# Kernel tuning notes

Measured on AMD Instinct MI355X. Metric: run time of the kernel, lower is better.

Reference implementation:

```python
import jax, jax.numpy as jnp
import numpy as np

DIM = 64
CTX = 64
HID = 512
K = 16          # n_bins
TB = 5.0        # tail_bound
N_T = DIM // 2  # n_transform_dims (mask_even=True -> odd indices transformed)
N_P = 3 * K - 1 # params per transformed dim
BATCH = 65536


def setup_inputs() -> dict:
    key = jax.random.key(0)
    ks = jax.random.split(key, 9)
    s = 0.05
    return {
        "x": jax.random.normal(ks[0], (BATCH, DIM), jnp.float32),
        "context": jax.random.normal(ks[1], (BATCH, CTX), jnp.float32),
        "W1": jax.random.normal(ks[2], (DIM + CTX, HID), jnp.float32) * s,
        "b1": jnp.zeros((HID,), jnp.float32),
        "W2": jax.random.normal(ks[3], (HID, HID), jnp.float32) * s,
        "b2": jnp.zeros((HID,), jnp.float32),
        "W3": jax.random.normal(ks[4], (HID, N_T * N_P), jnp.float32) * s,
        "b3": jnp.zeros((N_T * N_P,), jnp.float32),
    }


def _spline_forward(x, raw_params):
    # x: (batch, d); raw_params: (batch, d, 3K-1)
    B = TB
    Wb = jax.nn.softmax(raw_params[..., :K], axis=-1) * (2 * B)       # bin widths
    Hb = jax.nn.softmax(raw_params[..., K:2 * K], axis=-1) * (2 * B)  # bin heights
    D = jax.nn.softplus(raw_params[..., 2 * K:])                      # (batch,d,K-1)
    ones = jnp.ones(D.shape[:-1] + (1,), D.dtype)
    D = jnp.concatenate([ones, D, ones], axis=-1)                     # (batch,d,K+1)

    cumw = jnp.cumsum(Wb, axis=-1) - B
    cumh = jnp.cumsum(Hb, axis=-1) - B
    negB = jnp.full(cumw.shape[:-1] + (1,), -B, cumw.dtype)
    cumw = jnp.concatenate([negB, cumw], axis=-1)                     # (batch,d,K+1)
    cumh = jnp.concatenate([negB, cumh], axis=-1)

    x_c = jnp.clip(x, -B + 1e-06, B - 1e-06)
    # torch.searchsorted left on cumw[...,1:]: count of knots strictly < x
    bin_idx = jnp.sum(cumw[..., 1:] < x_c[..., None], axis=-1)
    bin_idx = jnp.clip(bin_idx, 0, K - 1)[..., None]                  # (batch,d,1)

    take = lambda a: jnp.take_along_axis(a, bin_idx, axis=-1)[..., 0]
    w_k = take(Wb)
    h_k = take(Hb)
    d_k = take(D[..., :-1])
    d_kp1 = take(D[..., 1:])
    cw_k = take(cumw)
    ch_k = take(cumh)

    xi = jnp.clip((x_c - cw_k) / w_k, 0.0, 1.0)
    om = 1.0 - xi
    numerator = h_k * (d_k * xi * xi + 2 * xi * om)
    denominator = d_k + (d_kp1 + d_k - 2) * xi * om
    y = ch_k + numerator / (denominator + 1e-08)
    log_deriv = jnp.log(
        h_k * h_k * (d_kp1 * xi * xi + 2 * xi * om + d_k * om * om)
        / (denominator * denominator * w_k + 1e-08) + 1e-08
    )
    return y, log_deriv


def reference(x, context, W1, b1, W2, b2, W3, b3):
    mask = jnp.zeros((DIM,), x.dtype).at[::2].set(1.0)
    x_masked = x * mask
    inp = jnp.concatenate([x_masked, context], axis=-1)
    h = jax.nn.silu(inp @ W1 + b1)
    h = jax.nn.silu(h @ W2 + b2)
    raw = (h @ W3 + b3).reshape(-1, N_T, N_P)
    x_t = x[:, 1::2]  # mask==0 columns (odd indices)
    y_t, log_det = _spline_forward(x_t, raw)
    y = x.at[:, 1::2].set(y_t)
    return y, jnp.sum(log_det, axis=-1)
```

## Files before the change

kernel.cpp:

```cpp
#include <hip/hip_runtime.h>


typedef _Float16 v8h __attribute__((ext_vector_type(8)));
typedef float v4f __attribute__((ext_vector_type(4)));

#define ROWS_PER_BLOCK 32
#define NBLOCKS (65536 / ROWS_PER_BLOCK)
#define NWAVES 16

#define SMEM_BYTES 147456
#define S_INPLO 8192
#define S_H1HI  16384
#define S_H1LO  49152
#define S_H2HI  81920
#define S_H2LO  114688
#define RAW_STRIDE 388

#define LO_SCALE 2048.f
#define LO_INV   (1.f / 2048.f)

__device__ __forceinline__ void split2(float x, _Float16& hi, _Float16& lo) {
    _Float16 h = (_Float16)x;
    hi = h;
    lo = (_Float16)((x - (float)h) * LO_SCALE);
}
__device__ __forceinline__ float silu_f(float v) {
    return v / (1.f + __expf(-v));
}
__device__ __forceinline__ float softplus_f(float v) {
    return v > 15.f ? v : __logf(1.f + __expf(v));
}

__global__ void nscl_prep_frag(const float* __restrict__ src,
                               _Float16* __restrict__ hi, _Float16* __restrict__ lo,
                               int K, int N) {
    int idx = blockIdx.x * blockDim.x + threadIdx.x;
    if (idx >= N * K) return;
    const int e    = idx & 7;
    const int lane = (idx >> 3) & 63;
    const int rem  = idx >> 9;
    const int KS   = K >> 5;
    const int ks   = rem % KS;
    const int j    = rem / KS;
    const int n = j * 16 + (lane & 15);
    const int k = ks * 32 + ((lane >> 4) << 3) + e;
    split2(src[k * N + n], hi[idx], lo[idx]);
}

template<int KS, int NPAIRS, bool DOSILU>
__device__ __forceinline__ void gemm_phase(const _Float16* __restrict__ sAhi,
                                           const _Float16* __restrict__ sAlo,
                                           const _Float16* __restrict__ Bhi,
                                           const _Float16* __restrict__ Blo,
                                           const float* __restrict__ bias,
                                           _Float16* __restrict__ sOutHi,
                                           _Float16* __restrict__ sOutLo,
                                           int wave, int lane) {
    const int lr = lane & 15;
    const int rb = (lane >> 4) << 2;

    for (int p = wave; p < NPAIRS; p += NWAVES) {
        const int j0 = p * 2;
        v4f m00 = {0,0,0,0}, m10 = {0,0,0,0}, m01 = {0,0,0,0}, m11 = {0,0,0,0};
        v4f c00 = {0,0,0,0}, c10 = {0,0,0,0}, c01 = {0,0,0,0}, c11 = {0,0,0,0};
        #pragma unroll
        for (int ks = 0; ks < KS; ++ks) {
            const int ab = (ks * 64 + lane) * 8;
            v8h a0h = *(const v8h*)(sAhi + ab);
            v8h a0l = *(const v8h*)(sAlo + ab);
            v8h a1h = *(const v8h*)(sAhi + KS * 512 + ab);
            v8h a1l = *(const v8h*)(sAlo + KS * 512 + ab);
            const int bo0 = ((j0 * KS + ks) * 64 + lane) * 8;
            const int bo1 = (((j0 + 1) * KS + ks) * 64 + lane) * 8;
            v8h b0h = *(const v8h*)(Bhi + bo0);
            v8h b0l = *(const v8h*)(Blo + bo0);
            v8h b1h = *(const v8h*)(Bhi + bo1);
            v8h b1l = *(const v8h*)(Blo + bo1);
            m00 = __builtin_amdgcn_mfma_f32_16x16x32_f16(a0h, b0h, m00, 0, 0, 0);
            m10 = __builtin_amdgcn_mfma_f32_16x16x32_f16(a1h, b0h, m10, 0, 0, 0);
            m01 = __builtin_amdgcn_mfma_f32_16x16x32_f16(a0h, b1h, m01, 0, 0, 0);
            m11 = __builtin_amdgcn_mfma_f32_16x16x32_f16(a1h, b1h, m11, 0, 0, 0);
            c00 = __builtin_amdgcn_mfma_f32_16x16x32_f16(a0h, b0l, c00, 0, 0, 0);
            c00 = __builtin_amdgcn_mfma_f32_16x16x32_f16(a0l, b0h, c00, 0, 0, 0);
            c10 = __builtin_amdgcn_mfma_f32_16x16x32_f16(a1h, b0l, c10, 0, 0, 0);
            c10 = __builtin_amdgcn_mfma_f32_16x16x32_f16(a1l, b0h, c10, 0, 0, 0);
            c01 = __builtin_amdgcn_mfma_f32_16x16x32_f16(a0h, b1l, c01, 0, 0, 0);
            c01 = __builtin_amdgcn_mfma_f32_16x16x32_f16(a0l, b1h, c01, 0, 0, 0);
            c11 = __builtin_amdgcn_mfma_f32_16x16x32_f16(a1h, b1l, c11, 0, 0, 0);
            c11 = __builtin_amdgcn_mfma_f32_16x16x32_f16(a1l, b1h, c11, 0, 0, 0);
        }
        #pragma unroll
        for (int jj = 0; jj < 2; ++jj) {
            const int C   = (j0 + jj) * 16 + lr;
            const int ks2 = C >> 5, g2 = (C >> 3) & 3, e2 = C & 7;
            const float bv = bias[C];
            const v4f mm0 = jj ? m01 : m00;
            const v4f mm1 = jj ? m11 : m10;
            const v4f cc0 = jj ? c01 : c00;
            const v4f cc1 = jj ? c11 : c10;
            #pragma unroll
            for (int r = 0; r < 4; ++r) {
                float v0 = mm0[r] + cc0[r] * LO_INV + bv;
                float v1 = mm1[r] + cc1[r] * LO_INV + bv;
                if (DOSILU) { v0 = silu_f(v0); v1 = silu_f(v1); }
                const int off0 = (ks2 * 64 + g2 * 16 + rb + r) * 8 + e2;
                const int off1 = ((16 + ks2) * 64 + g2 * 16 + rb + r) * 8 + e2;
                split2(v0, sOutHi[off0], sOutLo[off0]);
                split2(v1, sOutHi[off1], sOutLo[off1]);
            }
        }
    }
}

__device__ __forceinline__ void gemm3_chunk(const _Float16* __restrict__ sH2Hi,
                                            const _Float16* __restrict__ sH2Lo,
                                            const _Float16* __restrict__ W3hi,
                                            const _Float16* __restrict__ W3lo,
                                            const float* __restrict__ b3,
                                            float* __restrict__ sRaw,
                                            int t0, int wave, int lane) {
    const int lr = lane & 15;
    const int rb = (lane >> 4) << 2;

    for (int tt = wave; tt < 24; tt += NWAVES) {
        const int jt = t0 + tt;
        v4f m0 = {0,0,0,0}, m1 = {0,0,0,0};
        v4f cc0 = {0,0,0,0}, cc1 = {0,0,0,0};
        #pragma unroll
        for (int ks = 0; ks < 16; ++ks) {
            const int ab = (ks * 64 + lane) * 8;
            v8h a0h = *(const v8h*)(sH2Hi + ab);
            v8h a0l = *(const v8h*)(sH2Lo + ab);
            v8h a1h = *(const v8h*)(sH2Hi + 8192 + ab);
            v8h a1l = *(const v8h*)(sH2Lo + 8192 + ab);
            const int bo = ((jt * 16 + ks) * 64 + lane) * 8;
            v8h bh = *(const v8h*)(W3hi + bo);
            v8h bl = *(const v8h*)(W3lo + bo);
            m0  = __builtin_amdgcn_mfma_f32_16x16x32_f16(a0h, bh, m0, 0, 0, 0);
            m1  = __builtin_amdgcn_mfma_f32_16x16x32_f16(a1h, bh, m1, 0, 0, 0);
            cc0 = __builtin_amdgcn_mfma_f32_16x16x32_f16(a0h, bl, cc0, 0, 0, 0);
            cc0 = __builtin_amdgcn_mfma_f32_16x16x32_f16(a0l, bh, cc0, 0, 0, 0);
            cc1 = __builtin_amdgcn_mfma_f32_16x16x32_f16(a1h, bl, cc1, 0, 0, 0);
            cc1 = __builtin_amdgcn_mfma_f32_16x16x32_f16(a1l, bh, cc1, 0, 0, 0);
        }
        const int col  = jt * 16 + lr;
        const int lcol = tt * 16 + lr;
        const float bv = b3[col];
        #pragma unroll
        for (int r = 0; r < 4; ++r) {
            sRaw[(rb + r) * RAW_STRIDE + lcol]      = m0[r] + cc0[r] * LO_INV + bv;
            sRaw[(16 + rb + r) * RAW_STRIDE + lcol] = m1[r] + cc1[r] * LO_INV + bv;
        }
    }
}

__global__ __launch_bounds__(1024, 4)
void nscl_fused(const float* __restrict__ xp, const float* __restrict__ ctxp,
                const float* __restrict__ b1, const float* __restrict__ b2,
                const float* __restrict__ b3,
                const _Float16* __restrict__ W1Thi, const _Float16* __restrict__ W1Tlo,
                const _Float16* __restrict__ W2Thi, const _Float16* __restrict__ W2Tlo,
                const _Float16* __restrict__ W3Thi, const _Float16* __restrict__ W3Tlo,
                float* __restrict__ outY, float* __restrict__ outLD) {
    __shared__ __align__(16) char smem[SMEM_BYTES];
    _Float16* sInpHi = (_Float16*)smem;
    _Float16* sInpLo = (_Float16*)(smem + S_INPLO);
    _Float16* sH1Hi  = (_Float16*)(smem + S_H1HI);
    _Float16* sH1Lo  = (_Float16*)(smem + S_H1LO);
    _Float16* sH2Hi  = (_Float16*)(smem + S_H2HI);
    _Float16* sH2Lo  = (_Float16*)(smem + S_H2LO);
    float*    sRaw   = (float*)smem;

    const int tid  = threadIdx.x;
    const int lane = tid & 63;
    const int wave = tid >> 6;
    const int row0 = blockIdx.x * ROWS_PER_BLOCK;

    for (int idx = tid; idx < ROWS_PER_BLOCK * 128; idx += 1024) {
        const int e  = idx & 7;
        const int l  = (idx >> 3) & 63;
        const int ks = (idx >> 9) & 3;
        const int mt = idx >> 11;
        const int row = mt * 16 + (l & 15);
        const int c   = ks * 32 + ((l >> 4) << 3) + e;
        float v;
        if (c < 64) v = (c & 1) ? 0.f : xp[(row0 + row) * 64 + c];
        else        v = ctxp[(row0 + row) * 64 + (c - 64)];
        split2(v, sInpHi[idx], sInpLo[idx]);
    }
    __syncthreads();

    gemm_phase<4, 16, true>(sInpHi, sInpLo, W1Thi, W1Tlo, b1,
                            sH1Hi, sH1Lo, wave, lane);
    __syncthreads();
    gemm_phase<16, 16, true>(sH1Hi, sH1Lo, W2Thi, W2Tlo, b2,
                             sH2Hi, sH2Lo, wave, lane);
    __syncthreads();

    const float TB = 5.0f;
    float ldacc = 0.f;
    const int r  = (tid < 256) ? (tid >> 3) : 0;
    const int tl = tid & 7;
    const int t0s[4] = {0, 23, 47, 70};

    #pragma unroll 1
    for (int ch = 0; ch < 4; ++ch) {
        gemm3_chunk(sH2Hi, sH2Lo, W3Thi, W3Tlo, b3, sRaw, t0s[ch], wave, lane);
        __syncthreads();

        if (tid < 256) {
            const int t = ch * 8 + tl;
            const int g = row0 + r;
            const float* pr = sRaw + r * RAW_STRIDE + ((ch & 1) ? 8 : 0) + tl * 47;

            float mw = -1e30f, mh = -1e30f;
            #pragma unroll
            for (int i = 0; i < 16; ++i) {
                mw = fmaxf(mw, pr[i]);
                mh = fmaxf(mh, pr[16 + i]);
            }
            float wv[16], hv[16];
            float sw = 0.f, sh = 0.f;
            #pragma unroll
            for (int i = 0; i < 16; ++i) {
                wv[i] = __expf(pr[i] - mw);       sw += wv[i];
                hv[i] = __expf(pr[16 + i] - mh);  sh += hv[i];
            }
            const float scw = 10.f / sw;
            const float sch = 10.f / sh;

            const float xt = xp[g * 64 + 2 * t + 1];
            const float xc = fminf(fmaxf(xt, -TB + 1e-6f), TB - 1e-6f);

            float cum = -TB; int cnt = 0;
            #pragma unroll
            for (int i = 0; i < 16; ++i) {
                cum += wv[i] * scw;
                cnt += (cum < xc) ? 1 : 0;
            }
            const int bin = cnt > 15 ? 15 : cnt;

            float w_k = 0.f, cw_k = 0.f, h_k = 0.f, ch_k = 0.f;
            float cw = -TB, chh = -TB;
            #pragma unroll
            for (int i = 0; i < 16; ++i) {
                const float wi = wv[i] * scw;
                const float hi = hv[i] * sch;
                if (i == bin) { w_k = wi; cw_k = cw; h_k = hi; ch_k = chh; }
                cw += wi; chh += hi;
            }

            const float d_k  = (bin == 0)  ? 1.f : softplus_f(pr[31 + bin]);
            const float d_k1 = (bin == 15) ? 1.f : softplus_f(pr[32 + bin]);

            float xi = (xc - cw_k) / w_k;
            xi = fminf(fmaxf(xi, 0.f), 1.f);
            const float om = 1.f - xi;
            const float num = h_k * (d_k * xi * xi + 2.f * xi * om);
            const float den = d_k + (d_k1 + d_k - 2.f) * xi * om;
            const float yv  = ch_k + num / (den + 1e-8f);
            const float dv  = h_k * h_k * (d_k1 * xi * xi + 2.f * xi * om + d_k * om * om)
                              / (den * den * w_k + 1e-8f) + 1e-8f;

            float v = __logf(dv);
            v += __shfl_xor(v, 1);
            v += __shfl_xor(v, 2);
            v += __shfl_xor(v, 4);
            ldacc += v;

            outY[g * 64 + 2 * t]     = xp[g * 64 + 2 * t];
            outY[g * 64 + 2 * t + 1] = yv;
        }
        __syncthreads();
    }

    if (tid < 256 && tl == 0) outLD[row0 + r] = ldacc;
}

extern "C" void kernel_launch(void* const* d_in, const int* in_sizes, int n_in,
                              void* d_out, int out_size, void* d_ws, size_t ws_size,
                              hipStream_t stream) {
    (void)in_sizes; (void)n_in; (void)out_size; (void)ws_size;
    const float* x   = (const float*)d_in[0];
    const float* ctx = (const float*)d_in[1];
    const float* W1  = (const float*)d_in[2];
    const float* b1  = (const float*)d_in[3];
    const float* W2  = (const float*)d_in[4];
    const float* b2  = (const float*)d_in[5];
    const float* W3  = (const float*)d_in[6];
    const float* b3  = (const float*)d_in[7];

    _Float16* base = (_Float16*)d_ws;
    _Float16* W1Thi = base;
    _Float16* W1Tlo = base + 65536;
    _Float16* W2Thi = base + 131072;
    _Float16* W2Tlo = base + 393216;
    _Float16* W3Thi = base + 655360;
    _Float16* W3Tlo = base + 1425408;

    nscl_prep_frag<<<(512 * 128 + 255) / 256, 256, 0, stream>>>(W1, W1Thi, W1Tlo, 128, 512);
    nscl_prep_frag<<<(512 * 512 + 255) / 256, 256, 0, stream>>>(W2, W2Thi, W2Tlo, 512, 512);
    nscl_prep_frag<<<(512 * 1504 + 255) / 256, 256, 0, stream>>>(W3, W3Thi, W3Tlo, 512, 1504);

    float* outY  = (float*)d_out;
    float* outLD = outY + 65536 * 64;

    nscl_fused<<<NBLOCKS, 1024, 0, stream>>>(x, ctx, b1, b2, b3,
                                             W1Thi, W1Tlo, W2Thi, W2Tlo, W3Thi, W3Tlo,
                                             outY, outLD);
}
```

Baseline: 640.1 us.

## Use single-tile GEMM waves and recompute spline exps to cut register pressure

GEMM1/GEMM2 now give each wave one 16-column tile instead of a pair, halving accumulators and B-fragment registers per wave. Each B load is now reused across only two row tiles instead of four MFMA products, and all 32 tiles map onto 16 waves in two loop iterations. The spline stage no longer keeps 32-element exp arrays in registers and instead recomputes the exps in each pass, trading extra transcendental work for fewer live registers. The chunk offset table is replaced by an arithmetic expression that yields the same values.

```diff
diff --git a/kernel.cpp b/kernel.cpp
--- a/kernel.cpp
+++ b/kernel.cpp
@@ -3,6 +3,8 @@
 
 typedef _Float16 v8h __attribute__((ext_vector_type(8)));
 typedef float v4f __attribute__((ext_vector_type(4)));
+
+#define MFMA16(a, b, c) __builtin_amdgcn_mfma_f32_16x16x32_f16((a), (b), (c), 0, 0, 0)
 
 #define ROWS_PER_BLOCK 32
 #define NBLOCKS (65536 / ROWS_PER_BLOCK)
@@ -47,7 +49,7 @@
     split2(src[k * N + n], hi[idx], lo[idx]);
 }
 
-template<int KS, int NPAIRS, bool DOSILU>
+template<int KS, int NTILES, bool DOSILU>
 __device__ __forceinline__ void gemm_phase(const _Float16* __restrict__ sAhi,
                                            const _Float16* __restrict__ sAlo,
                                            const _Float16* __restrict__ Bhi,
@@ -59,10 +61,9 @@
     const int lr = lane & 15;
     const int rb = (lane >> 4) << 2;
 
-    for (int p = wave; p < NPAIRS; p += NWAVES) {
-        const int j0 = p * 2;
-        v4f m00 = {0,0,0,0}, m10 = {0,0,0,0}, m01 = {0,0,0,0}, m11 = {0,0,0,0};
-        v4f c00 = {0,0,0,0}, c10 = {0,0,0,0}, c01 = {0,0,0,0}, c11 = {0,0,0,0};
+    for (int p = wave; p < NTILES; p += NWAVES) {
+        v4f m0 = {0,0,0,0}, m1 = {0,0,0,0};
+        v4f c0 = {0,0,0,0}, c1 = {0,0,0,0};
         #pragma unroll
         for (int ks = 0; ks < KS; ++ks) {
             const int ab = (ks * 64 + lane) * 8;
@@ -70,44 +71,28 @@
             v8h a0l = *(const v8h*)(sAlo + ab);
             v8h a1h = *(const v8h*)(sAhi + KS * 512 + ab);
             v8h a1l = *(const v8h*)(sAlo + KS * 512 + ab);
-            const int bo0 = ((j0 * KS + ks) * 64 + lane) * 8;
-            const int bo1 = (((j0 + 1) * KS + ks) * 64 + lane) * 8;
-            v8h b0h = *(const v8h*)(Bhi + bo0);
-            v8h b0l = *(const v8h*)(Blo + bo0);
-            v8h b1h = *(const v8h*)(Bhi + bo1);
-            v8h b1l = *(const v8h*)(Blo + bo1);
-            m00 = __builtin_amdgcn_mfma_f32_16x16x32_f16(a0h, b0h, m00, 0, 0, 0);
-            m10 = __builtin_amdgcn_mfma_f32_16x16x32_f16(a1h, b0h, m10, 0, 0, 0);
-            m01 = __builtin_amdgcn_mfma_f32_16x16x32_f16(a0h, b1h, m01, 0, 0, 0);
-            m11 = __builtin_amdgcn_mfma_f32_16x16x32_f16(a1h, b1h, m11, 0, 0, 0);
-            c00 = __builtin_amdgcn_mfma_f32_16x16x32_f16(a0h, b0l, c00, 0, 0, 0);
-            c00 = __builtin_amdgcn_mfma_f32_16x16x32_f16(a0l, b0h, c00, 0, 0, 0);
-            c10 = __builtin_amdgcn_mfma_f32_16x16x32_f16(a1h, b0l, c10, 0, 0, 0);
-            c10 = __builtin_amdgcn_mfma_f32_16x16x32_f16(a1l, b0h, c10, 0, 0, 0);
-            c01 = __builtin_amdgcn_mfma_f32_16x16x32_f16(a0h, b1l, c01, 0, 0, 0);
-            c01 = __builtin_amdgcn_mfma_f32_16x16x32_f16(a0l, b1h, c01, 0, 0, 0);
-            c11 = __builtin_amdgcn_mfma_f32_16x16x32_f16(a1h, b1l, c11, 0, 0, 0);
-            c11 = __builtin_amdgcn_mfma_f32_16x16x32_f16(a1l, b1h, c11, 0, 0, 0);
-        }
-        #pragma unroll
-        for (int jj = 0; jj < 2; ++jj) {
-            const int C   = (j0 + jj) * 16 + lr;
-            const int ks2 = C >> 5, g2 = (C >> 3) & 3, e2 = C & 7;
-            const float bv = bias[C];
-            const v4f mm0 = jj ? m01 : m00;
-            const v4f mm1 = jj ? m11 : m10;
-            const v4f cc0 = jj ? c01 : c00;
-            const v4f cc1 = jj ? c11 : c10;
-            #pragma unroll
-            for (int r = 0; r < 4; ++r) {
-                float v0 = mm0[r] + cc0[r] * LO_INV + bv;
-                float v1 = mm1[r] + cc1[r] * LO_INV + bv;
-                if (DOSILU) { v0 = silu_f(v0); v1 = silu_f(v1); }
-                const int off0 = (ks2 * 64 + g2 * 16 + rb + r) * 8 + e2;
-                const int off1 = ((16 + ks2) * 64 + g2 * 16 + rb + r) * 8 + e2;
-                split2(v0, sOutHi[off0], sOutLo[off0]);
-                split2(v1, sOutHi[off1], sOutLo[off1]);
-            }
+            const int bo = ((p * KS + ks) * 64 + lane) * 8;
+            v8h bh = *(const v8h*)(Bhi + bo);
+            v8h bl = *(const v8h*)(Blo + bo);
+            m0 = MFMA16(a0h, bh, m0);
+            m1 = MFMA16(a1h, bh, m1);
+            c0 = MFMA16(a0h, bl, c0);
+            c0 = MFMA16(a0l, bh, c0);
+            c1 = MFMA16(a1h, bl, c1);
+            c1 = MFMA16(a1l, bh, c1);
+        }
+        const int C   = p * 16 + lr;
+        const int ks2 = C >> 5, g2 = (C >> 3) & 3, e2 = C & 7;
+        const float bv = bias[C];
+        #pragma unroll
+        for (int rr = 0; rr < 4; ++rr) {
+            float v0 = m0[rr] + c0[rr] * LO_INV + bv;
+            float v1 = m1[rr] + c1[rr] * LO_INV + bv;
+            if (DOSILU) { v0 = silu_f(v0); v1 = silu_f(v1); }
+            const int off0 = (ks2 * 64 + g2 * 16 + rb + rr) * 8 + e2;
+            const int off1 = ((16 + ks2) * 64 + g2 * 16 + rb + rr) * 8 + e2;
+            split2(v0, sOutHi[off0], sOutLo[off0]);
+            split2(v1, sOutHi[off1], sOutLo[off1]);
         }
     }
 }
@@ -125,7 +110,7 @@
     for (int tt = wave; tt < 24; tt += NWAVES) {
         const int jt = t0 + tt;
         v4f m0 = {0,0,0,0}, m1 = {0,0,0,0};
-        v4f cc0 = {0,0,0,0}, cc1 = {0,0,0,0};
+        v4f c0 = {0,0,0,0}, c1 = {0,0,0,0};
         #pragma unroll
         for (int ks = 0; ks < 16; ++ks) {
             const int ab = (ks * 64 + lane) * 8;
@@ -136,20 +121,20 @@
             const int bo = ((jt * 16 + ks) * 64 + lane) * 8;
             v8h bh = *(const v8h*)(W3hi + bo);
             v8h bl = *(const v8h*)(W3lo + bo);
-            m0  = __builtin_amdgcn_mfma_f32_16x16x32_f16(a0h, bh, m0, 0, 0, 0);
-            m1  = __builtin_amdgcn_mfma_f32_16x16x32_f16(a1h, bh, m1, 0, 0, 0);
-            cc0 = __builtin_amdgcn_mfma_f32_16x16x32_f16(a0h, bl, cc0, 0, 0, 0);
-            cc0 = __builtin_amdgcn_mfma_f32_16x16x32_f16(a0l, bh, cc0, 0, 0, 0);
-            cc1 = __builtin_amdgcn_mfma_f32_16x16x32_f16(a1h, bl, cc1, 0, 0, 0);
-            cc1 = __builtin_amdgcn_mfma_f32_16x16x32_f16(a1l, bh, cc1, 0, 0, 0);
+            m0 = MFMA16(a0h, bh, m0);
+            m1 = MFMA16(a1h, bh, m1);
+            c0 = MFMA16(a0h, bl, c0);
+            c0 = MFMA16(a0l, bh, c0);
+            c1 = MFMA16(a1h, bl, c1);
+            c1 = MFMA16(a1l, bh, c1);
         }
         const int col  = jt * 16 + lr;
         const int lcol = tt * 16 + lr;
         const float bv = b3[col];
         #pragma unroll
-        for (int r = 0; r < 4; ++r) {
-            sRaw[(rb + r) * RAW_STRIDE + lcol]      = m0[r] + cc0[r] * LO_INV + bv;
-            sRaw[(16 + rb + r) * RAW_STRIDE + lcol] = m1[r] + cc1[r] * LO_INV + bv;
+        for (int rr = 0; rr < 4; ++rr) {
+            sRaw[(rb + rr) * RAW_STRIDE + lcol]      = m0[rr] + c0[rr] * LO_INV + bv;
+            sRaw[(16 + rb + rr) * RAW_STRIDE + lcol] = m1[rr] + c1[rr] * LO_INV + bv;
         }
     }
 }
@@ -190,10 +175,10 @@
     }
     __syncthreads();
 
-    gemm_phase<4, 16, true>(sInpHi, sInpLo, W1Thi, W1Tlo, b1,
+    gemm_phase<4, 32, true>(sInpHi, sInpLo, W1Thi, W1Tlo, b1,
                             sH1Hi, sH1Lo, wave, lane);
     __syncthreads();
-    gemm_phase<16, 16, true>(sH1Hi, sH1Lo, W2Thi, W2Tlo, b2,
+    gemm_phase<16, 32, true>(sH1Hi, sH1Lo, W2Thi, W2Tlo, b2,
                              sH2Hi, sH2Lo, wave, lane);
     __syncthreads();
 
@@ -201,11 +186,11 @@
     float ldacc = 0.f;
     const int r  = (tid < 256) ? (tid >> 3) : 0;
     const int tl = tid & 7;
-    const int t0s[4] = {0, 23, 47, 70};
 
     #pragma unroll 1
     for (int ch = 0; ch < 4; ++ch) {
-        gemm3_chunk(sH2Hi, sH2Lo, W3Thi, W3Tlo, b3, sRaw, t0s[ch], wave, lane);
+        const int t0 = (ch * 47) >> 1;
+        gemm3_chunk(sH2Hi, sH2Lo, W3Thi, W3Tlo, b3, sRaw, t0, wave, lane);
         __syncthreads();
 
         if (tid < 256) {
@@ -219,12 +204,11 @@
                 mw = fmaxf(mw, pr[i]);
                 mh = fmaxf(mh, pr[16 + i]);
             }
-            float wv[16], hv[16];
             float sw = 0.f, sh = 0.f;
             #pragma unroll
             for (int i = 0; i < 16; ++i) {
-                wv[i] = __expf(pr[i] - mw);       sw += wv[i];
-                hv[i] = __expf(pr[16 + i] - mh);  sh += hv[i];
+                sw += __expf(pr[i] - mw);
+                sh += __expf(pr[16 + i] - mh);
             }
             const float scw = 10.f / sw;
             const float sch = 10.f / sh;
@@ -235,7 +219,7 @@
             float cum = -TB; int cnt = 0;
             #pragma unroll
             for (int i = 0; i < 16; ++i) {
-                cum += wv[i] * scw;
+                cum += __expf(pr[i] - mw) * scw;
                 cnt += (cum < xc) ? 1 : 0;
             }
             const int bin = cnt > 15 ? 15 : cnt;
@@ -244,8 +228,8 @@
             float cw = -TB, chh = -TB;
             #pragma unroll
             for (int i = 0; i < 16; ++i) {
-                const float wi = wv[i] * scw;
-                const float hi = hv[i] * sch;
+                const float wi = __expf(pr[i] - mw) * scw;
+                const float hi = __expf(pr[16 + i] - mh) * sch;
                 if (i == bin) { w_k = wi; cw_k = cw; h_k = hi; ch_k = chh; }
                 cw += wi; chh += hi;
             }
```

Result: slower. 2.228 ms (+248.0%).

## Switch third GEMM to 32x32x16 MFMA with matching fragment layouts

Applied to the files above, without the earlier changes.

The third GEMM now uses 32x32x16 MFMA tiles instead of pairs of 16x16x32 tiles. The W3 prep kernel and the second GEMM's output layout change to produce 32-wide fragments, and the chunking of columns into the raw scratch buffer is recomputed. The aim is fewer MFMA instructions and fewer operand loads per output. The trade-offs are a larger raw stride in shared memory, uneven tile counts per chunk, and more accumulator registers per wave.

```diff
diff --git a/kernel.cpp b/kernel.cpp
--- a/kernel.cpp
+++ b/kernel.cpp
@@ -3,6 +3,7 @@
 
 typedef _Float16 v8h __attribute__((ext_vector_type(8)));
 typedef float v4f __attribute__((ext_vector_type(4)));
+typedef float v16f __attribute__((ext_vector_type(16)));
 
 #define ROWS_PER_BLOCK 32
 #define NBLOCKS (65536 / ROWS_PER_BLOCK)
@@ -14,7 +15,7 @@
 #define S_H1LO  49152
 #define S_H2HI  81920
 #define S_H2LO  114688
-#define RAW_STRIDE 388
+#define RAW_STRIDE 420
 
 #define LO_SCALE 2048.f
 #define LO_INV   (1.f / 2048.f)
@@ -47,7 +48,23 @@
     split2(src[k * N + n], hi[idx], lo[idx]);
 }
 
-template<int KS, int NPAIRS, bool DOSILU>
+__global__ void nscl_prep_frag32(const float* __restrict__ src,
+                                 _Float16* __restrict__ hi, _Float16* __restrict__ lo,
+                                 int K, int N) {
+    int idx = blockIdx.x * blockDim.x + threadIdx.x;
+    if (idx >= N * K) return;
+    const int e    = idx & 7;
+    const int lane = (idx >> 3) & 63;
+    const int rem  = idx >> 9;
+    const int KK   = K >> 4;
+    const int kk   = rem % KK;
+    const int j    = rem / KK;
+    const int n = j * 32 + (lane & 31);
+    const int k = kk * 16 + ((lane >> 5) << 3) + e;
+    split2(src[k * N + n], hi[idx], lo[idx]);
+}
+
+template<int KS, int NPAIRS, bool DOSILU, bool OUT32>
 __device__ __forceinline__ void gemm_phase(const _Float16* __restrict__ sAhi,
                                            const _Float16* __restrict__ sAlo,
                                            const _Float16* __restrict__ Bhi,
@@ -91,8 +108,7 @@
         }
         #pragma unroll
         for (int jj = 0; jj < 2; ++jj) {
-            const int C   = (j0 + jj) * 16 + lr;
-            const int ks2 = C >> 5, g2 = (C >> 3) & 3, e2 = C & 7;
+            const int C = (j0 + jj) * 16 + lr;
             const float bv = bias[C];
             const v4f mm0 = jj ? m01 : m00;
             const v4f mm1 = jj ? m11 : m10;
@@ -103,8 +119,16 @@
                 float v0 = mm0[r] + cc0[r] * LO_INV + bv;
                 float v1 = mm1[r] + cc1[r] * LO_INV + bv;
                 if (DOSILU) { v0 = silu_f(v0); v1 = silu_f(v1); }
-                const int off0 = (ks2 * 64 + g2 * 16 + rb + r) * 8 + e2;
-                const int off1 = ((16 + ks2) * 64 + g2 * 16 + rb + r) * 8 + e2;
+                int off0, off1;
+                if (OUT32) {
+                    const int base = ((C >> 4) * 64 + 32 * ((C >> 3) & 1)) * 8 + (C & 7);
+                    off0 = base + (rb + r) * 8;
+                    off1 = base + (16 + rb + r) * 8;
+                } else {
+                    const int ks2 = C >> 5, g2 = (C >> 3) & 3, e2 = C & 7;
+                    off0 = (ks2 * 64 + g2 * 16 + rb + r) * 8 + e2;
+                    off1 = ((16 + ks2) * 64 + g2 * 16 + rb + r) * 8 + e2;
+                }
                 split2(v0, sOutHi[off0], sOutLo[off0]);
                 split2(v1, sOutHi[off1], sOutLo[off1]);
             }
@@ -112,44 +136,38 @@
     }
 }
 
-__device__ __forceinline__ void gemm3_chunk(const _Float16* __restrict__ sH2Hi,
-                                            const _Float16* __restrict__ sH2Lo,
-                                            const _Float16* __restrict__ W3hi,
-                                            const _Float16* __restrict__ W3lo,
-                                            const float* __restrict__ b3,
-                                            float* __restrict__ sRaw,
-                                            int t0, int wave, int lane) {
-    const int lr = lane & 15;
-    const int rb = (lane >> 4) << 2;
-
-    for (int tt = wave; tt < 24; tt += NWAVES) {
-        const int jt = t0 + tt;
-        v4f m0 = {0,0,0,0}, m1 = {0,0,0,0};
-        v4f cc0 = {0,0,0,0}, cc1 = {0,0,0,0};
+__device__ __forceinline__ void gemm3_chunk32(const _Float16* __restrict__ sH2Hi,
+                                              const _Float16* __restrict__ sH2Lo,
+                                              const _Float16* __restrict__ W3hi,
+                                              const _Float16* __restrict__ W3lo,
+                                              const float* __restrict__ b3,
+                                              float* __restrict__ sRaw,
+                                              int tstart, int ntiles,
+                                              int wave, int lane) {
+    for (int tt = wave; tt < ntiles; tt += NWAVES) {
+        const int jt = tstart + tt;
+        v16f m = {0,0,0,0,0,0,0,0,0,0,0,0,0,0,0,0};
+        v16f c = {0,0,0,0,0,0,0,0,0,0,0,0,0,0,0,0};
         #pragma unroll
-        for (int ks = 0; ks < 16; ++ks) {
-            const int ab = (ks * 64 + lane) * 8;
-            v8h a0h = *(const v8h*)(sH2Hi + ab);
-            v8h a0l = *(const v8h*)(sH2Lo + ab);
-            v8h a1h = *(const v8h*)(sH2Hi + 8192 + ab);
-            v8h a1l = *(const v8h*)(sH2Lo + 8192 + ab);
-            const int bo = ((jt * 16 + ks) * 64 + lane) * 8;
+        for (int kk = 0; kk < 32; ++kk) {
+            const int ab = (kk * 64 + lane) * 8;
+            v8h ah = *(const v8h*)(sH2Hi + ab);
+            v8h al = *(const v8h*)(sH2Lo + ab);
+            const int bo = ((jt * 32 + kk) * 64 + lane) * 8;
             v8h bh = *(const v8h*)(W3hi + bo);
             v8h bl = *(const v8h*)(W3lo + bo);
-            m0  = __builtin_amdgcn_mfma_f32_16x16x32_f16(a0h, bh, m0, 0, 0, 0);
-            m1  = __builtin_amdgcn_mfma_f32_16x16x32_f16(a1h, bh, m1, 0, 0, 0);
-            cc0 = __builtin_amdgcn_mfma_f32_16x16x32_f16(a0h, bl, cc0, 0, 0, 0);
-            cc0 = __builtin_amdgcn_mfma_f32_16x16x32_f16(a0l, bh, cc0, 0, 0, 0);
-            cc1 = __builtin_amdgcn_mfma_f32_16x16x32_f16(a1h, bl, cc1, 0, 0, 0);
-            cc1 = __builtin_amdgcn_mfma_f32_16x16x32_f16(a1l, bh, cc1, 0, 0, 0);
-        }
-        const int col  = jt * 16 + lr;
-        const int lcol = tt * 16 + lr;
-        const float bv = b3[col];
+            m = __builtin_amdgcn_mfma_f32_32x32x16_f16(ah, bh, m, 0, 0, 0);
+            c = __builtin_amdgcn_mfma_f32_32x32x16_f16(ah, bl, c, 0, 0, 0);
+            c = __builtin_amdgcn_mfma_f32_32x32x16_f16(al, bh, c, 0, 0, 0);
+        }
+        const int col32 = lane & 31;
+        const float bv = b3[jt * 32 + col32];
+        const int rbase = (lane >> 5) * 4;
+        const int lbase = tt * 32 + col32;
         #pragma unroll
-        for (int r = 0; r < 4; ++r) {
-            sRaw[(rb + r) * RAW_STRIDE + lcol]      = m0[r] + cc0[r] * LO_INV + bv;
-            sRaw[(16 + rb + r) * RAW_STRIDE + lcol] = m1[r] + cc1[r] * LO_INV + bv;
+        for (int r = 0; r < 16; ++r) {
+            const int row = (r & 3) + 8 * (r >> 2) + rbase;
+            sRaw[row * RAW_STRIDE + lbase] = m[r] + c[r] * LO_INV + bv;
         }
     }
 }
@@ -190,28 +208,31 @@
     }
     __syncthreads();
 
-    gemm_phase<4, 16, true>(sInpHi, sInpLo, W1Thi, W1Tlo, b1,
-                            sH1Hi, sH1Lo, wave, lane);
+    gemm_phase<4, 16, true, false>(sInpHi, sInpLo, W1Thi, W1Tlo, b1,
+                                   sH1Hi, sH1Lo, wave, lane);
     __syncthreads();
-    gemm_phase<16, 16, true>(sH1Hi, sH1Lo, W2Thi, W2Tlo, b2,
-                             sH2Hi, sH2Lo, wave, lane);
+    gemm_phase<16, 16, true, true>(sH1Hi, sH1Lo, W2Thi, W2Tlo, b2,
+                                   sH2Hi, sH2Lo, wave, lane);
     __syncthreads();
 
     const float TB = 5.0f;
     float ldacc = 0.f;
     const int r  = (tid < 256) ? (tid >> 3) : 0;
     const int tl = tid & 7;
-    const int t0s[4] = {0, 23, 47, 70};
 
     #pragma unroll 1
     for (int ch = 0; ch < 4; ++ch) {
-        gemm3_chunk(sH2Hi, sH2Lo, W3Thi, W3Tlo, b3, sRaw, t0s[ch], wave, lane);
+        const int tstart = (47 * ch) >> 2;
+        const int ntiles = ((376 * (ch + 1) + 31) >> 5) - tstart;
+        const int delta  = 376 * ch - 32 * tstart;
+        gemm3_chunk32(sH2Hi, sH2Lo, W3Thi, W3Tlo, b3, sRaw,
+                      tstart, ntiles, wave, lane);
         __syncthreads();
 
         if (tid < 256) {
             const int t = ch * 8 + tl;
             const int g = row0 + r;
-            const float* pr = sRaw + r * RAW_STRIDE + ((ch & 1) ? 8 : 0) + tl * 47;
+            const float* pr = sRaw + r * RAW_STRIDE + delta + tl * 47;
 
             float mw = -1e30f, mh = -1e30f;
             #pragma unroll
@@ -300,7 +321,7 @@
 
     nscl_prep_frag<<<(512 * 128 + 255) / 256, 256, 0, stream>>>(W1, W1Thi, W1Tlo, 128, 512);
     nscl_prep_frag<<<(512 * 512 + 255) / 256, 256, 0, stream>>>(W2, W2Thi, W2Tlo, 512, 512);
-    nscl_prep_frag<<<(512 * 1504 + 255) / 256, 256, 0, stream>>>(W3, W3Thi, W3Tlo, 512, 1504);
+    nscl_prep_frag32<<<(512 * 1504 + 255) / 256, 256, 0, stream>>>(W3, W3Thi, W3Tlo, 512, 1504);
 
     float* outY  = (float*)d_out;
     float* outLD = outY + 65536 * 64;
```

Measured after the change: 1.591 ms. +148.5%, slower.
